# Kernel tuning notes

Hardware: AMD Instinct MI355X
Metric: run time of the kernel (lower is better)

The kernel has to match this reference:

```python
import jax, jax.numpy as jnp
import numpy as np

HIDDEN = 128
N_RBF = 32
LMAX = 2
N_NODES = 10000
DEG = 8  # each node has DEG outgoing (and DEG incoming) edges on a ring


def _build_graph():
    src = np.repeat(np.arange(N_NODES, dtype=np.int64), DEG)
    offs = np.tile(np.arange(1, DEG + 1, dtype=np.int64), N_NODES)
    dst = (src + offs) % N_NODES
    keys = src * N_NODES + dst
    order = np.argsort(keys)
    src2, dst2 = src[order], dst[order]  # e2 sorted by key (searchsorted invariant)
    e1_to_e2 = np.empty_like(order)
    e1_to_e2[order] = np.arange(order.size)
    return src, dst, src2, dst2, e1_to_e2


def setup_inputs() -> dict:
    key = jax.random.key(0)
    ks = jax.random.split(key, 12)
    src1, dst1, src2, dst2, e1_to_e2 = _build_graph()
    E1, E2 = src1.size, src2.size
    in_dim = 6 * HIDDEN + 3 * N_RBF + 1  # 865

    def lin(k, fi, fo):
        kw, kb = jax.random.split(k)
        s = 1.0 / np.sqrt(fi)
        return (jax.random.uniform(kw, (fi, fo), minval=-s, maxval=s),
                jax.random.uniform(kb, (fo,), minval=-s, maxval=s))

    w1, b1 = lin(ks[0], in_dim, HIDDEN)
    w2, b2 = lin(ks[1], HIDDEN, HIDDEN)
    wgw, bgw = lin(ks[2], HIDDEN, HIDDEN)
    wgt, bgt = lin(ks[3], HIDDEN, HIDDEN)
    return {
        "t_e2": jax.random.normal(ks[4], (E2, HIDDEN), dtype=jnp.float32),
        "h": jax.random.normal(ks[5], (N_NODES, HIDDEN), dtype=jnp.float32),
        "edge_index1": jnp.asarray(np.stack([src1, dst1])),
        "edge_index2": jnp.asarray(np.stack([src2, dst2])),
        "e1_to_e2": jnp.asarray(e1_to_e2),
        "dist_e1": jax.random.uniform(ks[6], (E1,), dtype=jnp.float32),
        "dist_e2": jax.random.uniform(ks[7], (E2,), dtype=jnp.float32),
        "rbf_e1": jax.random.normal(ks[8], (E1, N_RBF), dtype=jnp.float32),
        "rbf_e2": jax.random.normal(ks[9], (E2, N_RBF), dtype=jnp.float32),
        "sph_e1": jax.random.normal(ks[10], (E1, LMAX + 1), dtype=jnp.float32),
        "num_nodes": N_NODES,
        "w1": w1, "b1": b1, "w2": w2, "b2": b2,
        "wgw": wgw, "bgw": bgw, "wgt": wgt, "bgt": bgt,
    }


def _wedge_indices(edge_index1, edge_index2, num_nodes):
    """Host-side (numpy, vectorized) wedge construction: for every center node k,
    all (incoming edge i->k, outgoing edge k->j) pairs with i != j, kept only when
    (i, j) itself is an edge in e2 (looked up by sorted key search)."""
    src1 = np.asarray(edge_index1[0]); dst1 = np.asarray(edge_index1[1])
    src2 = np.asarray(edge_index2[0]); dst2 = np.asarray(edge_index2[1])
    nz = src1 != dst1  # drop self-loops
    s, d = src1[nz], dst1[nz]
    eid = np.nonzero(nz)[0]
    out_deg = np.bincount(s, minlength=num_nodes)
    out_order = np.argsort(s, kind="stable")  # filtered-edge positions grouped by src
    out_ptr = np.concatenate([np.zeros(1, np.int64), np.cumsum(out_deg)])
    reps = out_deg[d]  # each incoming edge pairs with out_deg[center] outgoing edges
    total = int(reps.sum())
    if total == 0:
        z = np.zeros(0, np.int64)
        return z, z, z, z, z, z
    starts = np.cumsum(reps) - reps
    local = np.arange(total) - np.repeat(starts, reps)
    kj_f = out_order[np.repeat(out_ptr[d], reps) + local]
    i = np.repeat(s, reps)
    k = np.repeat(d, reps)
    eik = np.repeat(eid, reps)
    j = d[kj_f]
    ekj = eid[kj_f]
    m = i != j
    i, k, j, eik, ekj = i[m], k[m], j[m], eik[m], ekj[m]
    e2_keys = src2.astype(np.int64) * num_nodes + dst2
    pk = i.astype(np.int64) * num_nodes + j
    pos = np.searchsorted(e2_keys, pk)
    posc = np.minimum(pos, e2_keys.size - 1)
    valid = (pos < e2_keys.size) & (e2_keys[posc] == pk)
    return i[valid], k[valid], j[valid], eik[valid], ekj[valid], posc[valid]


def reference(t_e2, h, edge_index1, edge_index2, e1_to_e2, dist_e1, dist_e2,
              rbf_e1, rbf_e2, sph_e1, num_nodes,
              w1, b1, w2, b2, wgw, bgw, wgt, bgt):
    i, k, j, eik, ekj, eij = _wedge_indices(edge_index1, edge_index2, int(num_nodes))
    if i.size == 0:
        return t_e2
    i, k, j = jnp.asarray(i), jnp.asarray(k), jnp.asarray(j)
    eik, ekj, eij = jnp.asarray(eik), jnp.asarray(ekj), jnp.asarray(eij)
    e1e2 = jnp.asarray(e1_to_e2)
    # wedge geometric features (wedge_use_high_degree=False -> l=1 contraction only)
    c_feat = (sph_e1[eik, 1] * sph_e1[ekj, 1])[:, None]           # [W, 1]
    g = jnp.concatenate([rbf_e1[eik], rbf_e1[ekj], rbf_e2[eij], c_feat], axis=-1)
    rho_in = jnp.concatenate([t_e2[e1e2[eik]], t_e2[e1e2[ekj]], t_e2[eij],
                              h[i], h[k], h[j], g], axis=-1)       # [W, 865]
    msg = jax.nn.silu(rho_in @ w1 + b1) @ w2 + b2                  # [W, H]
    m = jax.ops.segment_sum(msg, eij, num_segments=t_e2.shape[0])  # [E2, H]
    return t_e2 + jax.nn.sigmoid(m @ wgw + bgw) * jnp.tanh(t_e2 @ wgt + bgt)
```

## Files before the change

### kernel.cpp

```cpp
#include <hip/hip_runtime.h>
#include <math.h>

typedef unsigned short u16;
typedef unsigned int u32;
typedef __bf16 bf16x8 __attribute__((ext_vector_type(8)));
typedef float f32x4 __attribute__((ext_vector_type(4)));

__device__ __forceinline__ float bf2f(u16 v){ union{u32 u;float f;}c; c.u=((u32)v)<<16; return c.f; }
__device__ __forceinline__ u16 f2bf(float f){ union{float f;u32 u;}c; c.f=f; u32 l=(c.u>>16)&1u; c.u+=0x7fffu+l; return (u16)(c.u>>16); }
__device__ __forceinline__ u32 pk2(float a, float b){ return (u32)f2bf(a) | ((u32)f2bf(b)<<16); }
__device__ __forceinline__ uint4 ld8f(const float* p){
  float4 x = ((const float4*)p)[0];
  float4 y = ((const float4*)p)[1];
  uint4 r; r.x=pk2(x.x,x.y); r.y=pk2(x.z,x.w); r.z=pk2(y.x,y.y); r.w=pk2(y.z,y.w);
  return r;
}
__device__ __forceinline__ float fsilu(float x){ return x/(1.f+__expf(-x)); }


__global__ void k_setup_edges(const int* __restrict__ e1_to_e2,
                              const float* __restrict__ rbf_e1,
                              const float* __restrict__ sph_e1,
                              u16* __restrict__ rbf1p,
                              float* __restrict__ sph_c, int E1) {
  int e = blockIdx.x*256 + threadIdx.x;
  if (e >= E1) return;
  int f = e1_to_e2[e];
  sph_c[f] = sph_e1[e*3+1];
  const float* s = rbf_e1 + (size_t)e*32;
  uint4* d = (uint4*)(rbf1p + (size_t)f*32);
  d[0]=ld8f(s); d[1]=ld8f(s+8); d[2]=ld8f(s+16); d[3]=ld8f(s+24);
}

__global__ void k_out_ptr(const int* __restrict__ src2, int* __restrict__ out_ptr,
                          int Nn, int E2) {
  int n = blockIdx.x*256 + threadIdx.x;
  if (n > Nn) return;
  int lo=0, hi=E2;
  while (lo<hi){ int m=(lo+hi)>>1; if (src2[m]<n) lo=m+1; else hi=m; }
  out_ptr[n]=lo;
}

__global__ void k_wbigt(const float* __restrict__ w1, u16* __restrict__ WbigT) {
  int id = blockIdx.x*256+threadIdx.x;
  if (id >= 384*448) return;
  int n = id/448, k = id%448;
  int q = n>>7, nn = n&127;
  int row = -1;
  if (k<128) row = q*128+k;
  else if (k<256) { if (q==0) row = 384+(k-128); }
  else if (k<384) { if (q==0) row = 512+(k-256); else if (q==1) row = 640+(k-256); }
  else if (k<416) { if (q==0) row = 768+(k-384); else if (q==1) row = 800+(k-384); }
  else { if (q==2) row = 832+(k-416); }
  WbigT[id] = (row>=0) ? f2bf(w1[row*128+nn]) : (u16)0;
}

__global__ void k_smallw(const float* __restrict__ w2, const float* __restrict__ wgw,
                         const float* __restrict__ wgt, const float* __restrict__ b2,
                         u16* __restrict__ WcT, u16* __restrict__ WgtT,
                         float* __restrict__ bc2) {
  int id = blockIdx.x*256+threadIdx.x;
  if (id < 16384) {
    int n = id&127, k = id>>7;
    float s = 0.f;
    for (int r=0;r<128;r++) s += w2[k*128+r]*wgw[r*128+n];
    WcT[n*128+k] = f2bf(s);
    WgtT[n*128+k] = f2bf(wgt[k*128+n]);
  } else if (id < 16384+128) {
    int n = id-16384;
    float s = 0.f;
    for (int r=0;r<128;r++) s += b2[r]*wgw[r*128+n];
    bc2[n] = s;
  }
}

__global__ __launch_bounds__(256, 8)
void k_enum(const int* __restrict__ src2, const int* __restrict__ dst2,
            const int* __restrict__ out_ptr, const float* __restrict__ sph_c,
            int4* __restrict__ wrec, int* __restrict__ cnt, int E2) {
  int id = blockIdx.x*256 + threadIdx.x;
  if (id >= E2*8) return;
  int gw = id >> 3, d = id & 7;
  int i = src2[gw], j = dst2[gw];
  int f = out_ptr[i] + d;
  if (f >= out_ptr[i+1]) return;
  int k = dst2[f];
  int lo = out_ptr[k], hi = out_ptr[k+1], hi0 = hi;
  while (lo<hi) { int m=(lo+hi)>>1; if (dst2[m]<j) lo=m+1; else hi=m; }
  if (lo < hi0 && dst2[lo]==j) {
    float cf = sph_c[f]*sph_c[lo];
    int slot = atomicAdd(&cnt[gw], 1);
    int4 r; r.x=f; r.y=lo; r.z=__float_as_int(cf); r.w=0;
    wrec[(size_t)gw*8 + slot] = r;
  }
}

__global__ __launch_bounds__(256, 8)
void k_wedge2(const u16* __restrict__ Q1, const u16* __restrict__ Q2,
              const u16* __restrict__ P3, const int4* __restrict__ wrec,
              const int* __restrict__ cnt, const float* __restrict__ w1,
              u16* __restrict__ S, int E2) {
  int gw = (int)((blockIdx.x*256 + threadIdx.x) >> 6);
  int lane = threadIdx.x & 63;
  if (gw >= E2) return;
  u32 p3u = ((const u32*)(P3 + (size_t)gw*128))[lane];
  float p30 = bf2f((u16)(p3u&0xffff)), p31 = bf2f((u16)(p3u>>16));
  float2 wv = ((const float2*)(w1 + 864*128))[lane];
  const u32* q1b = (const u32*)Q1;
  const u32* q2b = (const u32*)Q2;
  const int4* wr = wrec + (size_t)gw*8;
  int c = cnt[gw];
  float a0=0.f, a1=0.f;
  int w = 0;
  for (; w+2<=c; w+=2) {
    int4 rA = wr[w], rB = wr[w+1];
    u32 xA = q1b[(size_t)rA.x*64 + lane];
    u32 yA = q2b[(size_t)rA.y*64 + lane];
    u32 xB = q1b[(size_t)rB.x*64 + lane];
    u32 yB = q2b[(size_t)rB.y*64 + lane];
    float cfA = __int_as_float(rA.z), cfB = __int_as_float(rB.z);
    float x0 = p30 + bf2f((u16)(xA&0xffff)) + bf2f((u16)(yA&0xffff)) + cfA*wv.x;
    float x1 = p31 + bf2f((u16)(xA>>16))    + bf2f((u16)(yA>>16))    + cfA*wv.y;
    float z0 = p30 + bf2f((u16)(xB&0xffff)) + bf2f((u16)(yB&0xffff)) + cfB*wv.x;
    float z1 = p31 + bf2f((u16)(xB>>16))    + bf2f((u16)(yB>>16))    + cfB*wv.y;
    a0 += fsilu(x0) + fsilu(z0);
    a1 += fsilu(x1) + fsilu(z1);
  }
  if (w < c) {
    int4 rA = wr[w];
    u32 xA = q1b[(size_t)rA.x*64 + lane];
    u32 yA = q2b[(size_t)rA.y*64 + lane];
    float cfA = __int_as_float(rA.z);
    float x0 = p30 + bf2f((u16)(xA&0xffff)) + bf2f((u16)(yA&0xffff)) + cfA*wv.x;
    float x1 = p31 + bf2f((u16)(xA>>16))    + bf2f((u16)(yA>>16))    + cfA*wv.y;
    a0 += fsilu(x0);
    a1 += fsilu(x1);
  }
  ((u32*)(S + (size_t)gw*128))[lane] = pk2(a0, a1);
}

struct GArgs {
  const float* t_f32; const float* h; const float* rbf_e2;
  const u16* rbf1p; const u16* Asrc;
  const int* src2; const int* dst2; const int* cnt;
  const u16* Bmat; const u16* Gin;
  const float* b1; const float* bgw; const float* bgt; const float* bc2;
  u16* out0; u16* out1; u16* out2;
  float* outf;
  int M;
};

template<int MODE>
__global__ __launch_bounds__(256, 2)
void k_gemm(GArgs a) {
  constexpr int KT = (MODE==0)?448:128;
  constexpr int NK = KT/32;
  __shared__ u16 As[128*40];
  __shared__ u16 Bs[128*40];
  const int tid = threadIdx.x;
  const int bm = blockIdx.x, bn = blockIdx.y;
  const int lane = tid & 63, wave = tid >> 6;
  const int wm = wave >> 1, wn = wave & 1;
  const int quad = lane >> 4, l16 = lane & 15;

  const int part = tid & 3;
  const int ra = tid >> 2;
  const int rb = ra + 64;
  long fa = (long)bm*128 + ra;
  long fb = (long)bm*128 + rb;
  if (fa >= a.M) fa = a.M-1;
  if (fb >= a.M) fb = a.M-1;
  int sa=0, da=0, sb=0, db=0;
  if constexpr (MODE==0) { sa=a.src2[fa]; da=a.dst2[fa]; sb=a.src2[fb]; db=a.dst2[fb]; }

  f32x4 acc[4][4] = {};
  for (int ks=0; ks<NK; ks++) {
    const int kb = ks*32;
    uint4 va, vb;
    if constexpr (MODE==0) {
      if (ks<4)       { va = ld8f(a.t_f32 + fa*128 + kb + part*8);
                        vb = ld8f(a.t_f32 + fb*128 + kb + part*8); }
      else if (ks<8)  { va = ld8f(a.h + (long)sa*128 + (kb-128) + part*8);
                        vb = ld8f(a.h + (long)sb*128 + (kb-128) + part*8); }
      else if (ks<12) { va = ld8f(a.h + (long)da*128 + (kb-256) + part*8);
                        vb = ld8f(a.h + (long)db*128 + (kb-256) + part*8); }
      else if (ks==12){ va = *(const uint4*)(a.rbf1p + fa*32 + part*8);
                        vb = *(const uint4*)(a.rbf1p + fb*32 + part*8); }
      else            { va = ld8f(a.rbf_e2 + fa*32 + part*8);
                        vb = ld8f(a.rbf_e2 + fb*32 + part*8); }
    } else if constexpr (MODE==1) {
      va = *(const uint4*)(a.Asrc + fa*128 + kb + part*8);
      vb = *(const uint4*)(a.Asrc + fb*128 + kb + part*8);
    } else {
      va = ld8f(a.t_f32 + fa*128 + kb + part*8);
      vb = ld8f(a.t_f32 + fb*128 + kb + part*8);
    }
    uint4 wa = *(const uint4*)(a.Bmat + (long)(bn*128 + ra)*KT + kb + part*8);
    uint4 wb = *(const uint4*)(a.Bmat + (long)(bn*128 + rb)*KT + kb + part*8);
    __syncthreads();
    *(uint4*)(As + ra*40 + part*8) = va;
    *(uint4*)(As + rb*40 + part*8) = vb;
    *(uint4*)(Bs + ra*40 + part*8) = wa;
    *(uint4*)(Bs + rb*40 + part*8) = wb;
    __syncthreads();
    bf16x8 af[4], bfr[4];
    #pragma unroll
    for (int t=0;t<4;t++) {
      af[t]  = *(const bf16x8*)(As + (wm*64 + t*16 + l16)*40 + quad*8);
      bfr[t] = *(const bf16x8*)(Bs + (wn*64 + t*16 + l16)*40 + quad*8);
    }
    #pragma unroll
    for (int tm=0;tm<4;tm++)
      #pragma unroll
      for (int tn=0;tn<4;tn++)
        acc[tm][tn] = __builtin_amdgcn_mfma_f32_16x16x32_bf16(af[tm], bfr[tn], acc[tm][tn], 0,0,0);
  }

  #pragma unroll
  for (int tm=0;tm<4;tm++) {
    const int rloc = wm*64 + tm*16 + quad*4;
    #pragma unroll
    for (int r=0;r<4;r++) {
      long row = (long)bm*128 + rloc + r;
      if (row >= a.M) continue;
      #pragma unroll
      for (int tn=0;tn<4;tn++) {
        const int col = wn*64 + tn*16 + l16;
        float v = acc[tm][tn][r];
        if constexpr (MODE==0) {
          u16* dst = (bn==0)? a.out0 : (bn==1)? a.out1 : a.out2;
          if (bn==2) v += a.b1[col];
          dst[row*128 + col] = f2bf(v);
        } else if constexpr (MODE==1) {
          float u = v + (float)a.cnt[row]*a.bc2[col] + a.bgw[col];
          float g = 1.f/(1.f+__expf(-u));
          a.out0[row*128+col] = f2bf(g);
        } else {
          float vv = v + a.bgt[col];
          float th = 1.f - 2.f/(__expf(2.f*vv)+1.f);
          float t  = a.t_f32[row*128+col];
          float g  = bf2f(a.Gin[row*128+col]);
          a.outf[row*128+col] = t + g*th;
        }
      }
    }
  }
}

extern "C" void kernel_launch(void* const* d_in, const int* in_sizes, int n_in,
                              void* d_out, int out_size, void* d_ws, size_t ws_size,
                              hipStream_t stream) {
  const float* t_e2  = (const float*)d_in[0];
  const float* h     = (const float*)d_in[1];
  const int* ei2     = (const int*)d_in[3];
  const int* e1_to_e2 = (const int*)d_in[4];
  const float* rbf_e1 = (const float*)d_in[7];
  const float* rbf_e2 = (const float*)d_in[8];
  const float* sph_e1 = (const float*)d_in[9];
  const float* w1  = (const float*)d_in[11];
  const float* b1  = (const float*)d_in[12];
  const float* w2  = (const float*)d_in[13];
  const float* b2  = (const float*)d_in[14];
  const float* wgw = (const float*)d_in[15];
  const float* bgw = (const float*)d_in[16];
  const float* wgt = (const float*)d_in[17];
  const float* bgt = (const float*)d_in[18];

  const int E2 = in_sizes[0]/128;
  const int Nn = in_sizes[1]/128;
  const int E1 = in_sizes[5];
  const int* src2 = ei2;
  const int* dst2 = ei2 + E2;

  char* p = (char*)d_ws;
  u16* Q1 = (u16*)p;       p += (size_t)E2*128*2;
  u16* Q2 = (u16*)p;       p += (size_t)E2*128*2;
  u16* P3 = (u16*)p;       p += (size_t)E2*128*2;
  u16* rbf1p = (u16*)p;    p += (size_t)E2*32*2;
  u16* WbigT = (u16*)p;    p += (size_t)384*448*2;
  u16* WcT   = (u16*)p;    p += (size_t)128*128*2;
  u16* WgtT  = (u16*)p;    p += (size_t)128*128*2;
  float* sph_c = (float*)p; p += (size_t)E2*4;
  float* bc2   = (float*)p; p += 512;
  int* out_ptr = (int*)p;   p += (((size_t)(Nn+1)*4 + 63)/64)*64;
  int* cnt     = (int*)p;   p += (size_t)E2*4;
  int4* wrec   = (int4*)p;  p += (size_t)E2*8*16;
  u16* S = P3;
  u16* G = Q1;

  hipMemsetAsync(cnt, 0, (size_t)E2*4, stream);

  k_setup_edges<<<(E1+255)/256, 256, 0, stream>>>(e1_to_e2, rbf_e1, sph_e1, rbf1p, sph_c, E1);
  k_out_ptr<<<(Nn+1+255)/256, 256, 0, stream>>>(src2, out_ptr, Nn, E2);
  k_wbigt<<<(384*448+255)/256, 256, 0, stream>>>(w1, WbigT);
  k_smallw<<<(16512+255)/256, 256, 0, stream>>>(w2, wgw, wgt, b2, WcT, WgtT, bc2);
  k_enum<<<(E2*8+255)/256, 256, 0, stream>>>(src2, dst2, out_ptr, sph_c, wrec, cnt, E2);

  const int Mb = (E2+127)/128;
  {
    GArgs a = {};
    a.t_f32=t_e2; a.h=h; a.rbf1p=rbf1p; a.rbf_e2=rbf_e2;
    a.src2=src2; a.dst2=dst2; a.Bmat=WbigT; a.b1=b1;
    a.out0=Q1; a.out1=Q2; a.out2=P3; a.M=E2;
    k_gemm<0><<<dim3(Mb,3), 256, 0, stream>>>(a);
  }
  k_wedge2<<<(E2+3)/4, 256, 0, stream>>>(Q1, Q2, P3, wrec, cnt, w1, S, E2);
  {
    GArgs a = {};
    a.Asrc=S; a.cnt=cnt; a.Bmat=WcT; a.bgw=bgw; a.bc2=bc2;
    a.out0=G; a.M=E2;
    k_gemm<1><<<dim3(Mb,1), 256, 0, stream>>>(a);
  }
  {
    GArgs a = {};
    a.t_f32=t_e2; a.Bmat=WgtT; a.bgt=bgt; a.Gin=G;
    a.outf=(float*)d_out; a.M=E2;
    k_gemm<2><<<dim3(Mb,1), 256, 0, stream>>>(a);
  }
}
```

Before: 330.1 us.

## Merge setup kernels, pre-convert inputs to bf16, async double-buffer GEMMs, fuse gate GEMMs

The four setup kernels and the memset are merged into one multi-role launch, which also pre-converts t_e2, h and rbf_e2 to bf16. The GEMM kernel now loads tiles with global_load_lds into double-buffered shared memory, so the next k-step is fetched while MFMAs run, and the in-loop fp32-to-bf16 conversion is gone. The two final gate GEMMs (sigmoid branch and tanh branch) are fused into one kernel with two accumulator sets, which removes the intermediate G buffer and one launch. In exchange there is an extra pass that writes bf16 copies, more registers for the dual accumulators, and the residual now adds a bf16-rounded t instead of fp32, which could loosen accuracy.

```diff
diff --git a/kernel.cpp b/kernel.cpp
--- a/kernel.cpp
+++ b/kernel.cpp
@@ -17,60 +17,81 @@
 }
 __device__ __forceinline__ float fsilu(float x){ return x/(1.f+__expf(-x)); }
 
-
-__global__ void k_setup_edges(const int* __restrict__ e1_to_e2,
-                              const float* __restrict__ rbf_e1,
-                              const float* __restrict__ sph_e1,
-                              u16* __restrict__ rbf1p,
-                              float* __restrict__ sph_c, int E1) {
-  int e = blockIdx.x*256 + threadIdx.x;
-  if (e >= E1) return;
-  int f = e1_to_e2[e];
-  sph_c[f] = sph_e1[e*3+1];
-  const float* s = rbf_e1 + (size_t)e*32;
-  uint4* d = (uint4*)(rbf1p + (size_t)f*32);
-  d[0]=ld8f(s); d[1]=ld8f(s+8); d[2]=ld8f(s+16); d[3]=ld8f(s+24);
-}
-
-__global__ void k_out_ptr(const int* __restrict__ src2, int* __restrict__ out_ptr,
-                          int Nn, int E2) {
-  int n = blockIdx.x*256 + threadIdx.x;
-  if (n > Nn) return;
-  int lo=0, hi=E2;
-  while (lo<hi){ int m=(lo+hi)>>1; if (src2[m]<n) lo=m+1; else hi=m; }
-  out_ptr[n]=lo;
-}
-
-__global__ void k_wbigt(const float* __restrict__ w1, u16* __restrict__ WbigT) {
-  int id = blockIdx.x*256+threadIdx.x;
-  if (id >= 384*448) return;
-  int n = id/448, k = id%448;
-  int q = n>>7, nn = n&127;
-  int row = -1;
-  if (k<128) row = q*128+k;
-  else if (k<256) { if (q==0) row = 384+(k-128); }
-  else if (k<384) { if (q==0) row = 512+(k-256); else if (q==1) row = 640+(k-256); }
-  else if (k<416) { if (q==0) row = 768+(k-384); else if (q==1) row = 800+(k-384); }
-  else { if (q==2) row = 832+(k-416); }
-  WbigT[id] = (row>=0) ? f2bf(w1[row*128+nn]) : (u16)0;
-}
-
-__global__ void k_smallw(const float* __restrict__ w2, const float* __restrict__ wgw,
-                         const float* __restrict__ wgt, const float* __restrict__ b2,
-                         u16* __restrict__ WcT, u16* __restrict__ WgtT,
-                         float* __restrict__ bc2) {
-  int id = blockIdx.x*256+threadIdx.x;
-  if (id < 16384) {
-    int n = id&127, k = id>>7;
-    float s = 0.f;
-    for (int r=0;r<128;r++) s += w2[k*128+r]*wgw[r*128+n];
-    WcT[n*128+k] = f2bf(s);
-    WgtT[n*128+k] = f2bf(wgt[k*128+n]);
-  } else if (id < 16384+128) {
-    int n = id-16384;
-    float s = 0.f;
-    for (int r=0;r<128;r++) s += b2[r]*wgw[r*128+n];
-    bc2[n] = s;
+__device__ __forceinline__ void async16(const u16* g, u16* l) {
+  __builtin_amdgcn_global_load_lds(
+      (const __attribute__((address_space(1))) u32*)(g),
+      (__attribute__((address_space(3))) u32*)(l), 16, 0, 0);
+}
+
+struct SArgs {
+  const float *t, *h, *r2, *rbf_e1, *sph_e1, *w1, *w2, *wgw, *wgt, *b2;
+  const int *e1_to_e2, *src2;
+  u16 *T16, *h16, *rbf2b, *rbf1p, *WbigT, *WcT, *WgtT;
+  float *sph_c, *bc2;
+  int *out_ptr, *cnt;
+  long n_t, n_h, n_r;
+  int E1, E2, Nn;
+  int B0, B1, B2, B3, B4, B5;
+};
+
+__global__ __launch_bounds__(256)
+void k_setup(SArgs s) {
+  int b = blockIdx.x, tid = threadIdx.x;
+  if (b < s.B0) {
+    long base = ((long)b*256 + tid)*8;
+    if (base < s.n_t) {
+      *(uint4*)(s.T16+base) = ld8f(s.t+base);
+    } else if (base < s.n_t+s.n_h) {
+      long o = base-s.n_t;  *(uint4*)(s.h16+o) = ld8f(s.h+o);
+    } else if (base < s.n_t+s.n_h+s.n_r) {
+      long o = base-s.n_t-s.n_h; *(uint4*)(s.rbf2b+o) = ld8f(s.r2+o);
+    }
+  } else if (b < s.B1) {
+    int e = (b-s.B0)*256 + tid;
+    if (e < s.E1) {
+      int f = s.e1_to_e2[e];
+      s.sph_c[f] = s.sph_e1[e*3+1];
+      const float* src = s.rbf_e1 + (size_t)e*32;
+      uint4* d = (uint4*)(s.rbf1p + (size_t)f*32);
+      d[0]=ld8f(src); d[1]=ld8f(src+8); d[2]=ld8f(src+16); d[3]=ld8f(src+24);
+    }
+  } else if (b < s.B2) {
+    int n = (b-s.B1)*256 + tid;
+    if (n <= s.Nn) {
+      int lo=0, hi=s.E2;
+      while (lo<hi){ int m=(lo+hi)>>1; if (s.src2[m]<n) lo=m+1; else hi=m; }
+      s.out_ptr[n]=lo;
+    }
+  } else if (b < s.B3) {
+    int id = (b-s.B2)*256 + tid;
+    if (id < 384*448) {
+      int n = id/448, k = id%448;
+      int q = n>>7, nn = n&127;
+      int row = -1;
+      if (k<128) row = q*128+k;
+      else if (k<256) { if (q==0) row = 384+(k-128); }
+      else if (k<384) { if (q==0) row = 512+(k-256); else if (q==1) row = 640+(k-256); }
+      else if (k<416) { if (q==0) row = 768+(k-384); else if (q==1) row = 800+(k-384); }
+      else { if (q==2) row = 832+(k-416); }
+      s.WbigT[id] = (row>=0) ? f2bf(s.w1[row*128+nn]) : (u16)0;
+    }
+  } else if (b < s.B4) {
+    int id = (b-s.B3)*256 + tid;
+    if (id < 16384) {
+      int n = id&127, k = id>>7;
+      float acc = 0.f;
+      for (int r=0;r<128;r++) acc += s.w2[k*128+r]*s.wgw[r*128+n];
+      s.WcT[n*128+k] = f2bf(acc);
+      s.WgtT[n*128+k] = f2bf(s.wgt[k*128+n]);
+    } else if (id < 16384+128) {
+      int n = id-16384;
+      float acc = 0.f;
+      for (int r=0;r<128;r++) acc += s.b2[r]*s.wgw[r*128+n];
+      s.bc2[n] = acc;
+    }
+  } else if (b < s.B5) {
+    int e = (b-s.B4)*256 + tid;
+    if (e < s.E2) s.cnt[e] = 0;
   }
 }
 
@@ -140,12 +161,11 @@
 }
 
 struct GArgs {
-  const float* t_f32; const float* h; const float* rbf_e2;
-  const u16* rbf1p; const u16* Asrc;
-  const int* src2; const int* dst2; const int* cnt;
-  const u16* Bmat; const u16* Gin;
-  const float* b1; const float* bgw; const float* bgt; const float* bc2;
-  u16* out0; u16* out1; u16* out2;
+  const u16 *T16, *h16, *rbf1p, *rbf2b, *Asrc;
+  const int *src2, *dst2, *cnt;
+  const u16 *Bmat, *Bmat2;
+  const float *b1, *bgw, *bgt, *bc2;
+  u16 *out0, *out1, *out2;
   float* outf;
   int M;
 };
@@ -153,67 +173,76 @@
 template<int MODE>
 __global__ __launch_bounds__(256, 2)
 void k_gemm(GArgs a) {
-  constexpr int KT = (MODE==0)?448:128;
-  constexpr int NK = KT/32;
-  __shared__ u16 As[128*40];
-  __shared__ u16 Bs[128*40];
+  constexpr int NK = (MODE==0)?14:8;
+  constexpr int NA = (MODE==0)?1:2;
+  __shared__ u16 As[2][4096];
+  __shared__ u16 Bs[2][4096];
   const int tid = threadIdx.x;
-  const int bm = blockIdx.x, bn = blockIdx.y;
+  const int bm = blockIdx.x, bn = (MODE==0)? blockIdx.y : 0;
   const int lane = tid & 63, wave = tid >> 6;
   const int wm = wave >> 1, wn = wave & 1;
   const int quad = lane >> 4, l16 = lane & 15;
 
-  const int part = tid & 3;
-  const int ra = tid >> 2;
-  const int rb = ra + 64;
-  long fa = (long)bm*128 + ra;
-  long fb = (long)bm*128 + rb;
+  const int ar = (wave & 1)*64 + lane;
+  const int qh = wave >> 1;
+  long fa = (long)bm*128 + ar;
   if (fa >= a.M) fa = a.M-1;
-  if (fb >= a.M) fb = a.M-1;
-  int sa=0, da=0, sb=0, db=0;
-  if constexpr (MODE==0) { sa=a.src2[fa]; da=a.dst2[fa]; sb=a.src2[fb]; db=a.dst2[fb]; }
-
-  f32x4 acc[4][4] = {};
+
+  const u16 *tb, *hs, *hd, *r1, *r2;
+  if constexpr (MODE==0) {
+    int sa = a.src2[fa], da = a.dst2[fa];
+    tb = a.T16 + fa*128; hs = a.h16 + (long)sa*128; hd = a.h16 + (long)da*128;
+    r1 = a.rbf1p + fa*32; r2 = a.rbf2b + fa*32;
+  } else {
+    tb = a.Asrc + fa*128;
+    hs = a.T16 + fa*128;
+  }
+  auto agp = [&](int ks, int q) -> const u16* {
+    if constexpr (MODE==0) {
+      if (ks<4)   return tb + ks*32 + q*8;
+      if (ks<8)   return hs + (ks-4)*32 + q*8;
+      if (ks<12)  return hd + (ks-8)*32 + q*8;
+      if (ks==12) return r1 + q*8;
+      return r2 + q*8;
+    } else {
+      if (ks<4) return tb + ks*32 + q*8;
+      return hs + (ks-4)*32 + q*8;
+    }
+  };
+  const u16* Bb0; const u16* Bb1 = nullptr;
+  if constexpr (MODE==0) { Bb0 = a.Bmat + (long)(bn*128 + ar)*448; }
+  else { Bb0 = a.Bmat + (long)ar*128; Bb1 = a.Bmat2 + (long)ar*128; }
+  auto bgp = [&](int ks, int q) -> const u16* {
+    if constexpr (MODE==0) return Bb0 + ks*32 + q*8;
+    else return (ks<4) ? (Bb0 + ks*32 + q*8) : (Bb1 + (ks-4)*32 + q*8);
+  };
+  auto issue = [&](int ks, int buf) {
+    async16(agp(ks, qh),   As[buf] + wave*512);
+    async16(agp(ks, qh+2), As[buf] + (4+wave)*512);
+    async16(bgp(ks, qh),   Bs[buf] + wave*512);
+    async16(bgp(ks, qh+2), Bs[buf] + (4+wave)*512);
+  };
+
+  issue(0, 0);
+  __syncthreads();
+
+  f32x4 acc[NA][4][4] = {};
   for (int ks=0; ks<NK; ks++) {
-    const int kb = ks*32;
-    uint4 va, vb;
-    if constexpr (MODE==0) {
-      if (ks<4)       { va = ld8f(a.t_f32 + fa*128 + kb + part*8);
-                        vb = ld8f(a.t_f32 + fb*128 + kb + part*8); }
-      else if (ks<8)  { va = ld8f(a.h + (long)sa*128 + (kb-128) + part*8);
-                        vb = ld8f(a.h + (long)sb*128 + (kb-128) + part*8); }
-      else if (ks<12) { va = ld8f(a.h + (long)da*128 + (kb-256) + part*8);
-                        vb = ld8f(a.h + (long)db*128 + (kb-256) + part*8); }
-      else if (ks==12){ va = *(const uint4*)(a.rbf1p + fa*32 + part*8);
-                        vb = *(const uint4*)(a.rbf1p + fb*32 + part*8); }
-      else            { va = ld8f(a.rbf_e2 + fa*32 + part*8);
-                        vb = ld8f(a.rbf_e2 + fb*32 + part*8); }
-    } else if constexpr (MODE==1) {
-      va = *(const uint4*)(a.Asrc + fa*128 + kb + part*8);
-      vb = *(const uint4*)(a.Asrc + fb*128 + kb + part*8);
-    } else {
-      va = ld8f(a.t_f32 + fa*128 + kb + part*8);
-      vb = ld8f(a.t_f32 + fb*128 + kb + part*8);
-    }
-    uint4 wa = *(const uint4*)(a.Bmat + (long)(bn*128 + ra)*KT + kb + part*8);
-    uint4 wb = *(const uint4*)(a.Bmat + (long)(bn*128 + rb)*KT + kb + part*8);
-    __syncthreads();
-    *(uint4*)(As + ra*40 + part*8) = va;
-    *(uint4*)(As + rb*40 + part*8) = vb;
-    *(uint4*)(Bs + ra*40 + part*8) = wa;
-    *(uint4*)(Bs + rb*40 + part*8) = wb;
-    __syncthreads();
+    const int buf = ks & 1;
+    if (ks+1 < NK) issue(ks+1, buf^1);
+    const int sel = (NA==2) ? (ks>>2) : 0;
     bf16x8 af[4], bfr[4];
     #pragma unroll
     for (int t=0;t<4;t++) {
-      af[t]  = *(const bf16x8*)(As + (wm*64 + t*16 + l16)*40 + quad*8);
-      bfr[t] = *(const bf16x8*)(Bs + (wn*64 + t*16 + l16)*40 + quad*8);
+      af[t]  = *(const bf16x8*)(As[buf] + quad*1024 + (wm*64 + t*16 + l16)*8);
+      bfr[t] = *(const bf16x8*)(Bs[buf] + quad*1024 + (wn*64 + t*16 + l16)*8);
     }
     #pragma unroll
     for (int tm=0;tm<4;tm++)
       #pragma unroll
       for (int tn=0;tn<4;tn++)
-        acc[tm][tn] = __builtin_amdgcn_mfma_f32_16x16x32_bf16(af[tm], bfr[tn], acc[tm][tn], 0,0,0);
+        acc[sel][tm][tn] = __builtin_amdgcn_mfma_f32_16x16x32_bf16(af[tm], bfr[tn], acc[sel][tm][tn], 0,0,0);
+    __syncthreads();
   }
 
   #pragma unroll
@@ -226,20 +255,17 @@
       #pragma unroll
       for (int tn=0;tn<4;tn++) {
         const int col = wn*64 + tn*16 + l16;
-        float v = acc[tm][tn][r];
         if constexpr (MODE==0) {
+          float v = acc[0][tm][tn][r];
           u16* dst = (bn==0)? a.out0 : (bn==1)? a.out1 : a.out2;
           if (bn==2) v += a.b1[col];
           dst[row*128 + col] = f2bf(v);
-        } else if constexpr (MODE==1) {
-          float u = v + (float)a.cnt[row]*a.bc2[col] + a.bgw[col];
+        } else {
+          float u = acc[0][tm][tn][r] + (float)a.cnt[row]*a.bc2[col] + a.bgw[col];
           float g = 1.f/(1.f+__expf(-u));
-          a.out0[row*128+col] = f2bf(g);
-        } else {
-          float vv = v + a.bgt[col];
+          float vv = acc[1][tm][tn][r] + a.bgt[col];
           float th = 1.f - 2.f/(__expf(2.f*vv)+1.f);
-          float t  = a.t_f32[row*128+col];
-          float g  = bf2f(a.Gin[row*128+col]);
+          float t  = bf2f(a.T16[row*128+col]);
           a.outf[row*128+col] = t + g*th;
         }
       }
@@ -276,6 +302,9 @@
   u16* Q1 = (u16*)p;       p += (size_t)E2*128*2;
   u16* Q2 = (u16*)p;       p += (size_t)E2*128*2;
   u16* P3 = (u16*)p;       p += (size_t)E2*128*2;
+  u16* T16 = (u16*)p;      p += (size_t)E2*128*2;
+  u16* h16 = (u16*)p;      p += (size_t)Nn*128*2;
+  u16* rbf2b = (u16*)p;    p += (size_t)E2*32*2;
   u16* rbf1p = (u16*)p;    p += (size_t)E2*32*2;
   u16* WbigT = (u16*)p;    p += (size_t)384*448*2;
   u16* WcT   = (u16*)p;    p += (size_t)128*128*2;
@@ -286,20 +315,33 @@
   int* cnt     = (int*)p;   p += (size_t)E2*4;
   int4* wrec   = (int4*)p;  p += (size_t)E2*8*16;
   u16* S = P3;
-  u16* G = Q1;
-
-  hipMemsetAsync(cnt, 0, (size_t)E2*4, stream);
-
-  k_setup_edges<<<(E1+255)/256, 256, 0, stream>>>(e1_to_e2, rbf_e1, sph_e1, rbf1p, sph_c, E1);
-  k_out_ptr<<<(Nn+1+255)/256, 256, 0, stream>>>(src2, out_ptr, Nn, E2);
-  k_wbigt<<<(384*448+255)/256, 256, 0, stream>>>(w1, WbigT);
-  k_smallw<<<(16512+255)/256, 256, 0, stream>>>(w2, wgw, wgt, b2, WcT, WgtT, bc2);
+
+  long n_t = (long)E2*128, n_h = (long)Nn*128, n_r = (long)E2*32;
+  long tot8 = (n_t+n_h+n_r)/8;
+
+  SArgs s;
+  s.t=t_e2; s.h=h; s.r2=rbf_e2; s.rbf_e1=rbf_e1; s.sph_e1=sph_e1;
+  s.w1=w1; s.w2=w2; s.wgw=wgw; s.wgt=wgt; s.b2=b2;
+  s.e1_to_e2=e1_to_e2; s.src2=src2;
+  s.T16=T16; s.h16=h16; s.rbf2b=rbf2b; s.rbf1p=rbf1p;
+  s.WbigT=WbigT; s.WcT=WcT; s.WgtT=WgtT;
+  s.sph_c=sph_c; s.bc2=bc2; s.out_ptr=out_ptr; s.cnt=cnt;
+  s.n_t=n_t; s.n_h=n_h; s.n_r=n_r; s.E1=E1; s.E2=E2; s.Nn=Nn;
+  int B0 = (int)((tot8+255)/256);
+  int B1 = B0 + (E1+255)/256;
+  int B2 = B1 + (Nn+1+255)/256;
+  int B3 = B2 + (384*448+255)/256;
+  int B4 = B3 + (16512+255)/256;
+  int B5 = B4 + (E2+255)/256;
+  s.B0=B0; s.B1=B1; s.B2=B2; s.B3=B3; s.B4=B4; s.B5=B5;
+  k_setup<<<B5, 256, 0, stream>>>(s);
+
   k_enum<<<(E2*8+255)/256, 256, 0, stream>>>(src2, dst2, out_ptr, sph_c, wrec, cnt, E2);
 
   const int Mb = (E2+127)/128;
   {
     GArgs a = {};
-    a.t_f32=t_e2; a.h=h; a.rbf1p=rbf1p; a.rbf_e2=rbf_e2;
+    a.T16=T16; a.h16=h16; a.rbf1p=rbf1p; a.rbf2b=rbf2b;
     a.src2=src2; a.dst2=dst2; a.Bmat=WbigT; a.b1=b1;
     a.out0=Q1; a.out1=Q2; a.out2=P3; a.M=E2;
     k_gemm<0><<<dim3(Mb,3), 256, 0, stream>>>(a);
@@ -307,14 +349,9 @@
   k_wedge2<<<(E2+3)/4, 256, 0, stream>>>(Q1, Q2, P3, wrec, cnt, w1, S, E2);
   {
     GArgs a = {};
-    a.Asrc=S; a.cnt=cnt; a.Bmat=WcT; a.bgw=bgw; a.bc2=bc2;
-    a.out0=G; a.M=E2;
+    a.Asrc=S; a.T16=T16; a.cnt=cnt; a.Bmat=WcT; a.Bmat2=WgtT;
+    a.bgw=bgw; a.bgt=bgt; a.bc2=bc2;
+    a.outf=(float*)d_out; a.M=E2;
     k_gemm<1><<<dim3(Mb,1), 256, 0, stream>>>(a);
   }
-  {
-    GArgs a = {};
-    a.t_f32=t_e2; a.Bmat=WgtT; a.bgt=bgt; a.Gin=G;
-    a.outf=(float*)d_out; a.M=E2;
-    k_gemm<2><<<dim3(Mb,1), 256, 0, stream>>>(a);
-  }
-}
+}
```

Measured after the change: 340.1 us. 1.03x slower.
